# Kernel tuning notes

Measured on AMD Instinct MI355X. Metric: run time of the kernel, lower is better.

Reference implementation:

```python
import jax, jax.numpy as jnp
import numpy as np

N, F_IN, H, F_OUT = 8192, 256, 128, 16
POOL_RATIO = 0.5


def setup_inputs() -> dict:
    key = jax.random.key(0)
    ks = jax.random.split(key, 12)
    # Sparse-ish symmetric adjacency with zero diagonal (avg degree ~32).
    A = (jax.random.uniform(ks[0], (N, N)) < (32.0 / N)).astype(jnp.float32)
    A = jnp.maximum(A, A.T) * (1.0 - jnp.eye(N, dtype=jnp.float32))
    x = jax.random.normal(ks[1], (N, F_IN), dtype=jnp.float32)

    def lin(k, fin, fout):
        return (jax.random.normal(k, (fin, fout), dtype=jnp.float32) / np.float32(np.sqrt(fin)))

    return {
        "x": x, "A": A,
        "W0": lin(ks[2], F_IN, H), "b0": jnp.zeros((H,), jnp.float32),
        "W1": lin(ks[3], H, H),    "b1": jnp.zeros((H,), jnp.float32),
        "pw": lin(ks[4], H, 1),    "pb": jnp.zeros((1,), jnp.float32),
        "Wu": lin(ks[5], H, H),    "bu": jnp.zeros((H,), jnp.float32),
        "Wf": lin(ks[6], H, F_OUT), "bf": jnp.zeros((F_OUT,), jnp.float32),
    }


def _norm_adj(A):
    # normalize(): add self-loops (diag of A is 0), row-normalize D^-1 (A+I)
    Ah = A + jnp.eye(A.shape[0], dtype=A.dtype)
    r = jnp.sum(Ah, axis=1)
    r_inv = jnp.where(r > 0, 1.0 / r, 0.0)
    return Ah * r_inv[:, None]


def _gconv(x, A, W, b, act):
    h = x @ W + b          # nn.Linear
    h = _norm_adj(A) @ h   # spmm with row-normalized adjacency
    return act(h)


def reference(x, A, W0, b0, W1, b1, pw, pb, Wu, bu, Wf, bf):
    relu = jax.nn.relu
    ident = lambda t: t
    # down gconv 0
    h0 = _gconv(x, A, W0, b0, relu)                       # [N, H]
    # gPool: score -> l2-normalize -> sigmoid -> top-k gather
    score = h0 @ pw + pb                                  # [N, 1]
    score = score / jnp.sqrt(jnp.sum(score ** 2))
    score = jax.nn.sigmoid(score[:, 0])                   # [N]
    k = max(2, int(POOL_RATIO * h0.shape[0]))
    vals, idx = jax.lax.top_k(score, k)                   # [k]
    xp = h0[idx] * vals[:, None]                          # gated gather [k, H]
    Ap = A[idx][:, idx]                                   # pooled adjacency [k, k]
    # down gconv 1 (bottleneck, no pool after)
    h1 = _gconv(xp, Ap, W1, b1, relu)                     # [k, H]
    # gUnpool: zero-scatter back to N nodes
    xu = jnp.zeros((A.shape[0], h1.shape[1]), h1.dtype).at[idx].set(h1)
    # up gconv
    hu = _gconv(xu, A, Wu, bu, relu)                      # [N, H]
    # final gconv (identity activation) + log_softmax
    hf = _gconv(hu, A, Wf, bf, ident)                     # [N, F_OUT]
    return jax.nn.log_softmax(hf, axis=1)
```

## Files before the change

### kernel.cpp

```cpp
#include <hip/hip_runtime.h>
#include <math.h>

#define N_NODES 8192
#define FIN 256
#define HDIM 128
#define FOUTD 16
#define KSEL 4096
#define CAP 128

typedef unsigned int uint;
typedef unsigned short ushort;

static __device__ __forceinline__ ushort f2bf(float f) {
    uint u = __float_as_uint(f);
    return (ushort)((u + 0x7FFFu + ((u >> 16) & 1u)) >> 16);
}
static __device__ __forceinline__ float bf_lo(uint u) { return __uint_as_float(u << 16); }
static __device__ __forceinline__ float bf_hi(uint u) { return __uint_as_float(u & 0xFFFF0000u); }

__global__ __launch_bounds__(256) void csr_gemm0(const float* __restrict__ A,
                                                 int* __restrict__ cols,
                                                 int* __restrict__ deg,
                                                 const float* __restrict__ x,
                                                 const float* __restrict__ W0,
                                                 const float* __restrict__ b0,
                                                 float* __restrict__ T0) {
    int grp = blockIdx.x / 17;
    int rem = blockIdx.x - grp * 17;
    if (rem < 16) {
        int i = grp * 16 + rem;
        __shared__ int cnt;
        __shared__ int scols[CAP];
        if (threadIdx.x == 0) cnt = 0;
        __syncthreads();
        const float4* Arow = (const float4*)(A + (size_t)i * N_NODES);
        for (int c4 = threadIdx.x; c4 < N_NODES / 4; c4 += 256) {
            float4 v = Arow[c4];
            int base = c4 * 4;
            if (v.x != 0.0f) { int p = atomicAdd(&cnt, 1); if (p < CAP) scols[p] = base; }
            if (v.y != 0.0f) { int p = atomicAdd(&cnt, 1); if (p < CAP) scols[p] = base + 1; }
            if (v.z != 0.0f) { int p = atomicAdd(&cnt, 1); if (p < CAP) scols[p] = base + 2; }
            if (v.w != 0.0f) { int p = atomicAdd(&cnt, 1); if (p < CAP) scols[p] = base + 3; }
        }
        __syncthreads();
        int c = cnt; if (c > CAP) c = CAP;
        for (int t = threadIdx.x; t < c; t += 256)
            cols[(size_t)i * CAP + t] = scols[t];
        if (threadIdx.x == 0) deg[i] = c;
    } else {
        int half = threadIdx.x >> 7;
        int tid = threadIdx.x & 127;
        int row0 = grp * 16 + half * 8;
        float acc[8];
#pragma unroll
        for (int r = 0; r < 8; r++) acc[r] = 0.0f;
        const float* Xb = x + (size_t)row0 * FIN;
        for (int k = 0; k < FIN; k += 4) {
            float w0 = W0[(k + 0) * HDIM + tid];
            float w1 = W0[(k + 1) * HDIM + tid];
            float w2 = W0[(k + 2) * HDIM + tid];
            float w3 = W0[(k + 3) * HDIM + tid];
#pragma unroll
            for (int r = 0; r < 8; r++) {
                const float* xr = Xb + r * FIN + k;
                acc[r] = fmaf(xr[0], w0, acc[r]);
                acc[r] = fmaf(xr[1], w1, acc[r]);
                acc[r] = fmaf(xr[2], w2, acc[r]);
                acc[r] = fmaf(xr[3], w3, acc[r]);
            }
        }
        float bias = b0[tid];
#pragma unroll
        for (int r = 0; r < 8; r++)
            T0[(size_t)(row0 + r) * HDIM + tid] = acc[r] + bias;
    }
}

__global__ __launch_bounds__(128) void spmm_score(const float* __restrict__ T0,
                                                  const int* __restrict__ cols,
                                                  const int* __restrict__ deg,
                                                  const float* __restrict__ pw,
                                                  const float* __restrict__ pb,
                                                  float* __restrict__ H0,
                                                  float* __restrict__ sraw) {
    int wv = threadIdx.x >> 6, lane = threadIdx.x & 63;
    int row = blockIdx.x * 2 + wv;
    const float2* T2p = (const float2*)T0;
    const int* cl = cols + (size_t)row * CAP;
    int d = deg[row]; if (d > CAP) d = CAP;
    float2 a0 = {0.f, 0.f}, a1 = {0.f, 0.f}, a2 = {0.f, 0.f}, a3 = {0.f, 0.f};
    int j = 0;
    for (; j + 4 <= d; j += 4) {
        int c0 = cl[j], c1 = cl[j + 1], c2 = cl[j + 2], c3 = cl[j + 3];
        float2 v0 = T2p[(size_t)c0 * 64 + lane];
        float2 v1 = T2p[(size_t)c1 * 64 + lane];
        float2 v2 = T2p[(size_t)c2 * 64 + lane];
        float2 v3 = T2p[(size_t)c3 * 64 + lane];
        a0.x += v0.x; a0.y += v0.y;
        a1.x += v1.x; a1.y += v1.y;
        a2.x += v2.x; a2.y += v2.y;
        a3.x += v3.x; a3.y += v3.y;
    }
    for (; j < d; j++) {
        float2 v0 = T2p[(size_t)cl[j] * 64 + lane];
        a0.x += v0.x; a0.y += v0.y;
    }
    float2 own = T2p[(size_t)row * 64 + lane];
    float inv = 1.0f / (float)(1 + d);
    float hx = fmaxf((own.x + (a0.x + a1.x) + (a2.x + a3.x)) * inv, 0.f);
    float hy = fmaxf((own.y + (a0.y + a1.y) + (a2.y + a3.y)) * inv, 0.f);
    float2 h2; h2.x = hx; h2.y = hy;
    ((float2*)H0)[(size_t)row * 64 + lane] = h2;
    float2 pw2 = ((const float2*)pw)[lane];
    float v = hx * pw2.x + hy * pw2.y;
    for (int off = 32; off; off >>= 1) v += __shfl_down(v, off);
    if (lane == 0) sraw[row] = v + pb[0];
}

__global__ __launch_bounds__(256) void topk_radix(const float* __restrict__ sraw,
                                                  int* __restrict__ sel,
                                                  float* __restrict__ g) {
    int tid = threadIdx.x;
    int lane = tid & 63, wv = tid >> 6;
    float v[32];
    unsigned key[32];
    float ss = 0.f;
#pragma unroll
    for (int e = 0; e < 32; e++) {
        float x = sraw[tid * 32 + e];
        v[e] = x; ss += x * x;
        unsigned b = __float_as_uint(x);
        key[e] = (b & 0x80000000u) ? ~b : (b | 0x80000000u);
    }
    __shared__ float fr[4];
    for (int off = 32; off; off >>= 1) ss += __shfl_down(ss, off);
    if (lane == 0) fr[wv] = ss;
    __syncthreads();
    float inv_norm = 1.0f / sqrtf(fr[0] + fr[1] + fr[2] + fr[3]);

    __shared__ int hist[256];
    __shared__ int wred[4];
    __shared__ int bd, bkneed;
    unsigned prefix = 0; int kneed = KSEL;
    for (int pass = 0; pass < 4; pass++) {
        int shift = 24 - 8 * pass;
        unsigned maskAbove = (pass == 0) ? 0u : (0xFFFFFFFFu << (shift + 8));
        hist[tid] = 0;
        __syncthreads();
#pragma unroll
        for (int e = 0; e < 32; e++)
            if ((key[e] & maskAbove) == prefix)
                atomicAdd(&hist[(key[e] >> shift) & 255], 1);
        __syncthreads();
        int h = hist[tid];
        int s = h;
#pragma unroll
        for (int off = 1; off < 64; off <<= 1) {
            int t = __shfl_down(s, off);
            if (lane + off < 64) s += t;
        }
        if (lane == 0) wred[wv] = s;
        __syncthreads();
        int addhi = 0;
        for (int w = wv + 1; w < 4; w++) addhi += wred[w];
        int s_here = s + addhi;
        int s_next = s_here - h;
        if (s_here >= kneed && s_next < kneed) { bd = tid; bkneed = kneed - s_next; }
        __syncthreads();
        prefix |= ((unsigned)bd) << shift;
        kneed = bkneed;
        __syncthreads();
    }
    unsigned T = prefix;
    int eq = 0;
#pragma unroll
    for (int e = 0; e < 32; e++) eq += (key[e] == T);
    int p = eq;
#pragma unroll
    for (int off = 1; off < 64; off <<= 1) {
        int t = __shfl_up(p, off);
        if (lane >= off) p += t;
    }
    __shared__ int wpre[4];
    if (lane == 63) wpre[wv] = p;
    __syncthreads();
    int base = 0;
    for (int w = 0; w < wv; w++) base += wpre[w];
    int excl = base + p - eq;
    int seen = 0;
#pragma unroll
    for (int e = 0; e < 32; e++) {
        int i = tid * 32 + e;
        int s2;
        if (key[e] > T) s2 = 1;
        else if (key[e] == T) { s2 = (excl + seen < kneed) ? 1 : 0; seen++; }
        else s2 = 0;
        sel[i] = s2;
        g[i] = s2 ? (1.0f / (1.0f + expf(-(v[e] * inv_norm)))) : 0.0f;
    }
}

__global__ __launch_bounds__(128) void gemm1(const float* __restrict__ X,
                                             const float* __restrict__ W,
                                             const float* __restrict__ b,
                                             const float* __restrict__ scale,
                                             ushort* __restrict__ Y) {
    int tid = threadIdx.x;
    int row0 = blockIdx.x * 8;
    float acc[8];
#pragma unroll
    for (int r = 0; r < 8; r++) acc[r] = 0.0f;
    const float* Xb = X + (size_t)row0 * HDIM;
    for (int k = 0; k < HDIM; k += 4) {
        float w0 = W[(k + 0) * HDIM + tid];
        float w1 = W[(k + 1) * HDIM + tid];
        float w2 = W[(k + 2) * HDIM + tid];
        float w3 = W[(k + 3) * HDIM + tid];
#pragma unroll
        for (int r = 0; r < 8; r++) {
            const float* xr = Xb + r * HDIM + k;
            acc[r] = fmaf(xr[0], w0, acc[r]);
            acc[r] = fmaf(xr[1], w1, acc[r]);
            acc[r] = fmaf(xr[2], w2, acc[r]);
            acc[r] = fmaf(xr[3], w3, acc[r]);
        }
    }
    float bias = b[tid];
#pragma unroll
    for (int r = 0; r < 8; r++) {
        float val = fmaf(acc[r], scale[row0 + r], bias);
        Y[(size_t)(row0 + r) * HDIM + tid] = f2bf(val);
    }
}

__global__ __launch_bounds__(64) void pool_gemm(const uint* __restrict__ T1u,
                                                const int* __restrict__ cols,
                                                const int* __restrict__ deg,
                                                const int* __restrict__ sel,
                                                const float* __restrict__ Wu,
                                                const float* __restrict__ bu,
                                                uint* __restrict__ T2u) {
    int row = blockIdx.x;
    int t = threadIdx.x;
    float2 bias = ((const float2*)bu)[t];
    if (!sel[row]) {
        T2u[(size_t)row * 64 + t] = (uint)f2bf(bias.x) | ((uint)f2bf(bias.y) << 16);
        return;
    }
    const int* cl = cols + (size_t)row * CAP;
    int d = deg[row]; if (d > CAP) d = CAP;
    uint su = T1u[(size_t)row * 64 + t];
    float ax = bf_lo(su), ay = bf_hi(su);
    int cnt = 0;
    for (int j = 0; j < d; j++) {
        int c = cl[j];
        if (sel[c]) {
            cnt++;
            uint u = T1u[(size_t)c * 64 + t];
            ax += bf_lo(u); ay += bf_hi(u);
        }
    }
    float inv = 1.0f / (float)(1 + cnt);
    float xux = fmaxf(ax * inv, 0.f);
    float xuy = fmaxf(ay * inv, 0.f);
    float accx = bias.x, accy = bias.y;
    const float2* Wur = (const float2*)Wu;
#pragma unroll 4
    for (int kk = 0; kk < 64; kk++) {
        float xk0 = __uint_as_float(__builtin_amdgcn_readlane(__float_as_uint(xux), kk));
        float xk1 = __uint_as_float(__builtin_amdgcn_readlane(__float_as_uint(xuy), kk));
        float2 w0 = Wur[(size_t)(2 * kk) * 64 + t];
        float2 w1 = Wur[(size_t)(2 * kk + 1) * 64 + t];
        accx = fmaf(xk0, w0.x, accx); accy = fmaf(xk0, w0.y, accy);
        accx = fmaf(xk1, w1.x, accx); accy = fmaf(xk1, w1.y, accy);
    }
    T2u[(size_t)row * 64 + t] = (uint)f2bf(accx) | ((uint)f2bf(accy) << 16);
}

__global__ __launch_bounds__(64) void up_gemm16(const uint* __restrict__ T2u,
                                                const int* __restrict__ cols,
                                                const int* __restrict__ deg,
                                                const float* __restrict__ Wf,
                                                const float* __restrict__ bf_,
                                                float* __restrict__ T3) {
    int row = blockIdx.x;
    int t = threadIdx.x;
    const int* cl = cols + (size_t)row * CAP;
    int d = deg[row]; if (d > CAP) d = CAP;
    uint su = T2u[(size_t)row * 64 + t];
    float ax = bf_lo(su), ay = bf_hi(su);
    for (int j = 0; j < d; j++) {
        uint u = T2u[(size_t)cl[j] * 64 + t];
        ax += bf_lo(u); ay += bf_hi(u);
    }
    float inv = 1.0f / (float)(1 + d);
    float hux = fmaxf(ax * inv, 0.f);
    float huy = fmaxf(ay * inv, 0.f);
    __shared__ float hs[128];
    hs[2 * t] = hux; hs[2 * t + 1] = huy;
    __syncthreads();
    int c = t & 15, gg = t >> 4;
    float p = 0.f;
#pragma unroll 8
    for (int kk = 0; kk < 32; kk++) {
        int k = gg * 32 + kk;
        p = fmaf(hs[k], Wf[k * FOUTD + c], p);
    }
    p += __shfl_xor(p, 16);
    p += __shfl_xor(p, 32);
    if (t < 16) T3[(size_t)row * FOUTD + t] = p + bf_[t];
}

__global__ __launch_bounds__(64) void spmm16_lsm(const float* __restrict__ T3,
                                                 const int* __restrict__ cols,
                                                 const int* __restrict__ deg,
                                                 float* __restrict__ out) {
    int lane = threadIdx.x;
    int r = lane >> 4, c = lane & 15;
    int row = blockIdx.x * 4 + r;
    const int* cl = cols + (size_t)row * CAP;
    int d = deg[row]; if (d > CAP) d = CAP;
    float acc = T3[(size_t)row * FOUTD + c];
    for (int j = 0; j < d; j++) acc += T3[(size_t)cl[j] * FOUTD + c];
    float v = acc / (float)(1 + d);
    float m = v;
    for (int off = 1; off < 16; off <<= 1) m = fmaxf(m, __shfl_xor(m, off, 16));
    float e = expf(v - m);
    float s = e;
    for (int off = 1; off < 16; off <<= 1) s += __shfl_xor(s, off, 16);
    out[(size_t)row * FOUTD + c] = v - m - logf(s);
}

extern "C" void kernel_launch(void* const* d_in, const int* in_sizes, int n_in,
                              void* d_out, int out_size, void* d_ws, size_t ws_size,
                              hipStream_t stream) {
    const float* x  = (const float*)d_in[0];
    const float* A  = (const float*)d_in[1];
    const float* W0 = (const float*)d_in[2];
    const float* b0 = (const float*)d_in[3];
    const float* W1 = (const float*)d_in[4];
    const float* b1 = (const float*)d_in[5];
    const float* pw = (const float*)d_in[6];
    const float* pb = (const float*)d_in[7];
    const float* Wu = (const float*)d_in[8];
    const float* bu = (const float*)d_in[9];
    const float* Wf = (const float*)d_in[10];
    const float* bf = (const float*)d_in[11];
    float* out = (float*)d_out;

    char* ws = (char*)d_ws;
    const size_t MB = 1024 * 1024;
    int*   cols = (int*)  (ws);
    int*   deg  = (int*)  (ws + 4  * MB);
    float* T0   = (float*)(ws + 5  * MB);
    float* H0   = (float*)(ws + 9  * MB);
    uint*  T1   = (uint*) (ws + 13 * MB);
    uint*  T2   = (uint*) (ws + 15 * MB);
    float* T3   = (float*)(ws + 17 * MB);
    float* sraw = (float*)(ws + 18 * MB);
    int*   sel  = (int*)  (ws + 18 * MB + 512 * 1024);
    float* g    = (float*)(ws + 19 * MB);

    csr_gemm0<<<512 * 17, 256, 0, stream>>>(A, cols, deg, x, W0, b0, T0);
    spmm_score<<<N_NODES / 2, 128, 0, stream>>>(T0, cols, deg, pw, pb, H0, sraw);
    topk_radix<<<1, 256, 0, stream>>>(sraw, sel, g);
    gemm1<<<N_NODES / 8, 128, 0, stream>>>(H0, W1, b1, g, (ushort*)T1);
    pool_gemm<<<N_NODES, 64, 0, stream>>>(T1, cols, deg, sel, Wu, bu, T2);
    up_gemm16<<<N_NODES, 64, 0, stream>>>(T2, cols, deg, Wf, bf, T3);
    spmm16_lsm<<<N_NODES / 4, 64, 0, stream>>>(T3, cols, deg, out);
}
```

Baseline: 583.2 us.

## Exploit adjacency symmetry to halve CSR scan and fold W1 GEMM before pooling

The CSR build now reads only the upper triangle of each adjacency row and a new mirror kernel fills the lower-triangle entries with global atomics, relying on A being symmetric. The W1 projection is computed inside the first spmm kernel before gating, with the gate and bias applied during pooled aggregation, removing the separate gemm1 kernel and the H0 buffer. This cuts the dominant dense adjacency read roughly in half and removes a launch and an intermediate round-trip. It assumes a symmetric input and makes neighbour order nondeterministic.

After: 596.5 us. 2.3% more time.

```diff
diff --git a/kernel.cpp b/kernel.cpp
--- a/kernel.cpp
+++ b/kernel.cpp
@@ -18,13 +18,14 @@
 static __device__ __forceinline__ float bf_lo(uint u) { return __uint_as_float(u << 16); }
 static __device__ __forceinline__ float bf_hi(uint u) { return __uint_as_float(u & 0xFFFF0000u); }
 
-__global__ __launch_bounds__(256) void csr_gemm0(const float* __restrict__ A,
-                                                 int* __restrict__ cols,
-                                                 int* __restrict__ deg,
-                                                 const float* __restrict__ x,
-                                                 const float* __restrict__ W0,
-                                                 const float* __restrict__ b0,
-                                                 float* __restrict__ T0) {
+__global__ __launch_bounds__(256) void csru_gemm0(const float* __restrict__ A,
+                                                  int* __restrict__ cols,
+                                                  int* __restrict__ degU,
+                                                  int* __restrict__ degT,
+                                                  const float* __restrict__ x,
+                                                  const float* __restrict__ W0,
+                                                  const float* __restrict__ b0,
+                                                  float* __restrict__ T0) {
     int grp = blockIdx.x / 17;
     int rem = blockIdx.x - grp * 17;
     if (rem < 16) {
@@ -34,19 +35,19 @@
         if (threadIdx.x == 0) cnt = 0;
         __syncthreads();
         const float4* Arow = (const float4*)(A + (size_t)i * N_NODES);
-        for (int c4 = threadIdx.x; c4 < N_NODES / 4; c4 += 256) {
+        for (int c4 = (i >> 2) + threadIdx.x; c4 < N_NODES / 4; c4 += 256) {
             float4 v = Arow[c4];
             int base = c4 * 4;
-            if (v.x != 0.0f) { int p = atomicAdd(&cnt, 1); if (p < CAP) scols[p] = base; }
-            if (v.y != 0.0f) { int p = atomicAdd(&cnt, 1); if (p < CAP) scols[p] = base + 1; }
-            if (v.z != 0.0f) { int p = atomicAdd(&cnt, 1); if (p < CAP) scols[p] = base + 2; }
-            if (v.w != 0.0f) { int p = atomicAdd(&cnt, 1); if (p < CAP) scols[p] = base + 3; }
+            if (v.x != 0.0f && base + 0 > i) { int p = atomicAdd(&cnt, 1); if (p < CAP) scols[p] = base; }
+            if (v.y != 0.0f && base + 1 > i) { int p = atomicAdd(&cnt, 1); if (p < CAP) scols[p] = base + 1; }
+            if (v.z != 0.0f && base + 2 > i) { int p = atomicAdd(&cnt, 1); if (p < CAP) scols[p] = base + 2; }
+            if (v.w != 0.0f && base + 3 > i) { int p = atomicAdd(&cnt, 1); if (p < CAP) scols[p] = base + 3; }
         }
         __syncthreads();
         int c = cnt; if (c > CAP) c = CAP;
         for (int t = threadIdx.x; t < c; t += 256)
             cols[(size_t)i * CAP + t] = scols[t];
-        if (threadIdx.x == 0) deg[i] = c;
+        if (threadIdx.x == 0) { degU[i] = c; degT[i] = c; }
     } else {
         int half = threadIdx.x >> 7;
         int tid = threadIdx.x & 127;
@@ -76,18 +77,32 @@
     }
 }
 
-__global__ __launch_bounds__(128) void spmm_score(const float* __restrict__ T0,
-                                                  const int* __restrict__ cols,
-                                                  const int* __restrict__ deg,
-                                                  const float* __restrict__ pw,
-                                                  const float* __restrict__ pb,
-                                                  float* __restrict__ H0,
-                                                  float* __restrict__ sraw) {
+__global__ __launch_bounds__(256) void csr_mirror(int* __restrict__ cols,
+                                                  const int* __restrict__ degU,
+                                                  int* __restrict__ degT) {
+    int wv = threadIdx.x >> 6, lane = threadIdx.x & 63;
+    int i = blockIdx.x * 4 + wv;
+    int du = degU[i];
+    for (int t = lane; t < du; t += 64) {
+        int j = cols[(size_t)i * CAP + t];
+        int pos = atomicAdd(&degT[j], 1);
+        if (pos < CAP) cols[(size_t)j * CAP + pos] = i;
+    }
+}
+
+__global__ __launch_bounds__(128) void spmm_score_p1(const float* __restrict__ T0,
+                                                     const int* __restrict__ cols,
+                                                     const int* __restrict__ degT,
+                                                     const float* __restrict__ pw,
+                                                     const float* __restrict__ pb,
+                                                     const float* __restrict__ W1,
+                                                     uint* __restrict__ P1u,
+                                                     float* __restrict__ sraw) {
     int wv = threadIdx.x >> 6, lane = threadIdx.x & 63;
     int row = blockIdx.x * 2 + wv;
     const float2* T2p = (const float2*)T0;
     const int* cl = cols + (size_t)row * CAP;
-    int d = deg[row]; if (d > CAP) d = CAP;
+    int d = degT[row]; if (d > CAP) d = CAP;
     float2 a0 = {0.f, 0.f}, a1 = {0.f, 0.f}, a2 = {0.f, 0.f}, a3 = {0.f, 0.f};
     int j = 0;
     for (; j + 4 <= d; j += 4) {
@@ -109,12 +124,22 @@
     float inv = 1.0f / (float)(1 + d);
     float hx = fmaxf((own.x + (a0.x + a1.x) + (a2.x + a3.x)) * inv, 0.f);
     float hy = fmaxf((own.y + (a0.y + a1.y) + (a2.y + a3.y)) * inv, 0.f);
-    float2 h2; h2.x = hx; h2.y = hy;
-    ((float2*)H0)[(size_t)row * 64 + lane] = h2;
     float2 pw2 = ((const float2*)pw)[lane];
     float v = hx * pw2.x + hy * pw2.y;
     for (int off = 32; off; off >>= 1) v += __shfl_down(v, off);
     if (lane == 0) sraw[row] = v + pb[0];
+    float accx = 0.f, accy = 0.f;
+    const float2* W1r = (const float2*)W1;
+#pragma unroll 4
+    for (int kk = 0; kk < 64; kk++) {
+        float xk0 = __uint_as_float(__builtin_amdgcn_readlane(__float_as_uint(hx), kk));
+        float xk1 = __uint_as_float(__builtin_amdgcn_readlane(__float_as_uint(hy), kk));
+        float2 w0 = W1r[(size_t)(2 * kk) * 64 + lane];
+        float2 w1 = W1r[(size_t)(2 * kk + 1) * 64 + lane];
+        accx = fmaf(xk0, w0.x, accx); accy = fmaf(xk0, w0.y, accy);
+        accx = fmaf(xk1, w1.x, accx); accy = fmaf(xk1, w1.y, accy);
+    }
+    P1u[(size_t)row * 64 + lane] = (uint)f2bf(accx) | ((uint)f2bf(accy) << 16);
 }
 
 __global__ __launch_bounds__(256) void topk_radix(const float* __restrict__ sraw,
@@ -200,70 +225,42 @@
     }
 }
 
-__global__ __launch_bounds__(128) void gemm1(const float* __restrict__ X,
-                                             const float* __restrict__ W,
-                                             const float* __restrict__ b,
-                                             const float* __restrict__ scale,
-                                             ushort* __restrict__ Y) {
-    int tid = threadIdx.x;
-    int row0 = blockIdx.x * 8;
-    float acc[8];
-#pragma unroll
-    for (int r = 0; r < 8; r++) acc[r] = 0.0f;
-    const float* Xb = X + (size_t)row0 * HDIM;
-    for (int k = 0; k < HDIM; k += 4) {
-        float w0 = W[(k + 0) * HDIM + tid];
-        float w1 = W[(k + 1) * HDIM + tid];
-        float w2 = W[(k + 2) * HDIM + tid];
-        float w3 = W[(k + 3) * HDIM + tid];
-#pragma unroll
-        for (int r = 0; r < 8; r++) {
-            const float* xr = Xb + r * HDIM + k;
-            acc[r] = fmaf(xr[0], w0, acc[r]);
-            acc[r] = fmaf(xr[1], w1, acc[r]);
-            acc[r] = fmaf(xr[2], w2, acc[r]);
-            acc[r] = fmaf(xr[3], w3, acc[r]);
-        }
-    }
-    float bias = b[tid];
-#pragma unroll
-    for (int r = 0; r < 8; r++) {
-        float val = fmaf(acc[r], scale[row0 + r], bias);
-        Y[(size_t)(row0 + r) * HDIM + tid] = f2bf(val);
-    }
-}
-
-__global__ __launch_bounds__(64) void pool_gemm(const uint* __restrict__ T1u,
+__global__ __launch_bounds__(64) void pool_gemm(const uint* __restrict__ P1u,
                                                 const int* __restrict__ cols,
-                                                const int* __restrict__ deg,
+                                                const int* __restrict__ degT,
                                                 const int* __restrict__ sel,
+                                                const float* __restrict__ g,
+                                                const float* __restrict__ b1,
                                                 const float* __restrict__ Wu,
                                                 const float* __restrict__ bu,
                                                 uint* __restrict__ T2u) {
     int row = blockIdx.x;
     int t = threadIdx.x;
-    float2 bias = ((const float2*)bu)[t];
+    float2 biasU = ((const float2*)bu)[t];
     if (!sel[row]) {
-        T2u[(size_t)row * 64 + t] = (uint)f2bf(bias.x) | ((uint)f2bf(bias.y) << 16);
+        T2u[(size_t)row * 64 + t] = (uint)f2bf(biasU.x) | ((uint)f2bf(biasU.y) << 16);
         return;
     }
     const int* cl = cols + (size_t)row * CAP;
-    int d = deg[row]; if (d > CAP) d = CAP;
-    uint su = T1u[(size_t)row * 64 + t];
-    float ax = bf_lo(su), ay = bf_hi(su);
+    int d = degT[row]; if (d > CAP) d = CAP;
+    uint su = P1u[(size_t)row * 64 + t];
+    float grow = g[row];
+    float ax = bf_lo(su) * grow, ay = bf_hi(su) * grow;
     int cnt = 0;
     for (int j = 0; j < d; j++) {
         int c = cl[j];
         if (sel[c]) {
             cnt++;
-            uint u = T1u[(size_t)c * 64 + t];
-            ax += bf_lo(u); ay += bf_hi(u);
+            uint u = P1u[(size_t)c * 64 + t];
+            float gc = g[c];
+            ax = fmaf(bf_lo(u), gc, ax); ay = fmaf(bf_hi(u), gc, ay);
         }
     }
+    float2 b1p = ((const float2*)b1)[t];
     float inv = 1.0f / (float)(1 + cnt);
-    float xux = fmaxf(ax * inv, 0.f);
-    float xuy = fmaxf(ay * inv, 0.f);
-    float accx = bias.x, accy = bias.y;
+    float xux = fmaxf(fmaf(ax, inv, b1p.x), 0.f);
+    float xuy = fmaxf(fmaf(ay, inv, b1p.y), 0.f);
+    float accx = biasU.x, accy = biasU.y;
     const float2* Wur = (const float2*)Wu;
 #pragma unroll 4
     for (int kk = 0; kk < 64; kk++) {
@@ -279,14 +276,14 @@
 
 __global__ __launch_bounds__(64) void up_gemm16(const uint* __restrict__ T2u,
                                                 const int* __restrict__ cols,
-                                                const int* __restrict__ deg,
+                                                const int* __restrict__ degT,
                                                 const float* __restrict__ Wf,
                                                 const float* __restrict__ bf_,
                                                 float* __restrict__ T3) {
     int row = blockIdx.x;
     int t = threadIdx.x;
     const int* cl = cols + (size_t)row * CAP;
-    int d = deg[row]; if (d > CAP) d = CAP;
+    int d = degT[row]; if (d > CAP) d = CAP;
     uint su = T2u[(size_t)row * 64 + t];
     float ax = bf_lo(su), ay = bf_hi(su);
     for (int j = 0; j < d; j++) {
@@ -313,13 +310,13 @@
 
 __global__ __launch_bounds__(64) void spmm16_lsm(const float* __restrict__ T3,
                                                  const int* __restrict__ cols,
-                                                 const int* __restrict__ deg,
+                                                 const int* __restrict__ degT,
                                                  float* __restrict__ out) {
     int lane = threadIdx.x;
     int r = lane >> 4, c = lane & 15;
     int row = blockIdx.x * 4 + r;
     const int* cl = cols + (size_t)row * CAP;
-    int d = deg[row]; if (d > CAP) d = CAP;
+    int d = degT[row]; if (d > CAP) d = CAP;
     float acc = T3[(size_t)row * FOUTD + c];
     for (int j = 0; j < d; j++) acc += T3[(size_t)cl[j] * FOUTD + c];
     float v = acc / (float)(1 + d);
@@ -351,21 +348,21 @@
     char* ws = (char*)d_ws;
     const size_t MB = 1024 * 1024;
     int*   cols = (int*)  (ws);
-    int*   deg  = (int*)  (ws + 4  * MB);
+    int*   degU = (int*)  (ws + 4 * MB);
+    int*   degT = (int*)  (ws + 4 * MB + 65536);
     float* T0   = (float*)(ws + 5  * MB);
-    float* H0   = (float*)(ws + 9  * MB);
-    uint*  T1   = (uint*) (ws + 13 * MB);
-    uint*  T2   = (uint*) (ws + 15 * MB);
-    float* T3   = (float*)(ws + 17 * MB);
-    float* sraw = (float*)(ws + 18 * MB);
-    int*   sel  = (int*)  (ws + 18 * MB + 512 * 1024);
-    float* g    = (float*)(ws + 19 * MB);
-
-    csr_gemm0<<<512 * 17, 256, 0, stream>>>(A, cols, deg, x, W0, b0, T0);
-    spmm_score<<<N_NODES / 2, 128, 0, stream>>>(T0, cols, deg, pw, pb, H0, sraw);
+    uint*  P1   = (uint*) (ws + 9  * MB);
+    uint*  T2   = (uint*) (ws + 11 * MB);
+    float* T3   = (float*)(ws + 13 * MB);
+    float* sraw = (float*)(ws + 14 * MB);
+    int*   sel  = (int*)  (ws + 14 * MB + 65536);
+    float* g    = (float*)(ws + 14 * MB + 131072);
+
+    csru_gemm0<<<512 * 17, 256, 0, stream>>>(A, cols, degU, degT, x, W0, b0, T0);
+    csr_mirror<<<N_NODES / 4, 256, 0, stream>>>(cols, degU, degT);
+    spmm_score_p1<<<N_NODES / 2, 128, 0, stream>>>(T0, cols, degT, pw, pb, W1, P1, sraw);
     topk_radix<<<1, 256, 0, stream>>>(sraw, sel, g);
-    gemm1<<<N_NODES / 8, 128, 0, stream>>>(H0, W1, b1, g, (ushort*)T1);
-    pool_gemm<<<N_NODES, 64, 0, stream>>>(T1, cols, deg, sel, Wu, bu, T2);
-    up_gemm16<<<N_NODES, 64, 0, stream>>>(T2, cols, deg, Wf, bf, T3);
-    spmm16_lsm<<<N_NODES / 4, 64, 0, stream>>>(T3, cols, deg, out);
-}
+    pool_gemm<<<N_NODES, 64, 0, stream>>>(P1, cols, degT, sel, g, b1, Wu, bu, T2);
+    up_gemm16<<<N_NODES, 64, 0, stream>>>(T2, cols, degT, Wf, bf, T3);
+    spmm16_lsm<<<N_NODES / 4, 64, 0, stream>>>(T3, cols, degT, out);
+}
```
